# Performance work log

Hardware: AMD Instinct MI355X
Metric: run time of the kernel (lower is better)

Reference implementation:

```python
import jax, jax.numpy as jnp
import numpy as np

B, L, D = 4, 2048, 768
H, K = 12, 9
IPG = D // H  # in-channels per group = head_size = 64
PAD = (K - 1) // 2


def setup_inputs() -> dict:
    key = jax.random.key(0)
    ks = jax.random.split(key, 8)
    s = lambda k, shape, scale: jax.random.normal(k, shape, dtype=jnp.float32) * scale
    return {
        "query": s(ks[0], (B, L, D), 1.0),
        "dw_w": s(ks[1], (D, 1, K), 0.1),          # depthwise Conv1d weight, no bias
        "pw_w": s(ks[2], (H, IPG, IPG), 0.05),     # grouped 1x1 conv [head, out_pg, in_pg]
        "pw_b": s(ks[3], (D,), 0.02),
        "ak_w": s(ks[4], (H, K, IPG), 0.05),       # conv_attn_kernel grouped 1x1 [head, K, in_pg]
        "ak_b": s(ks[5], (H * K,), 0.02),
        "pt_w": s(ks[6], (D, D), 0.02),            # conv_attn_point Linear weight [out, in]
        "pt_b": s(ks[7], (D,), 0.02),
    }


def _sdconv(query, dw_w, pw_w, pw_b, ak_w, ak_b, pt_w, pt_b):
    b, l, d = query.shape
    # SeparableConv1d: depthwise conv (groups=D, kernel K, padding PAD, no bias)
    x = query.transpose(0, 2, 1)  # [B, D, L]
    dw = jax.lax.conv_general_dilated(
        x, dw_w, window_strides=(1,), padding=[(PAD, PAD)],
        feature_group_count=d, dimension_numbers=("NCH", "OIH", "NCH"))  # [B, D, L]
    # grouped pointwise conv (groups=H, kernel 1)
    dwg = dw.reshape(b, H, IPG, l)
    pw = jnp.einsum("bhil,hoi->bhol", dwg, pw_w).reshape(b, d, l) + pw_b[None, :, None]
    key_conv_attn = pw.transpose(0, 2, 1)  # [B, L, D]
    # stride == 1 path: elementwise gate with query
    conv_attn = key_conv_attn * query  # [B, L, D]
    # conv_attn_kernel: grouped 1x1 conv D -> H*K (per head: IPG -> K)
    ca = conv_attn.reshape(b, l, H, IPG)
    kern = jnp.einsum("blhi,hki->blhk", ca, ak_w) + ak_b.reshape(H, K)  # [B, L, H, K]
    w = jax.nn.softmax(kern, axis=-1)  # softmax over kernel positions
    # conv_attn_point linear on value (= query here)
    v = query @ pt_w.T + pt_b  # [B, L, D]
    # unfold: local windows of size K around each position
    vp = jnp.pad(v, ((0, 0), (PAD, PAD), (0, 0)))
    idx = jnp.arange(l)[:, None] + jnp.arange(K)[None, :]  # [L, K]
    win = vp[:, idx]  # [B, L, K, D]
    winh = win.reshape(b, l, K, H, IPG)
    out = jnp.einsum("blkhd,blhk->blhd", winh, w).reshape(b, l, d)
    return out


def reference(query, dw_w, pw_w, pw_b, ak_w, ak_b, pt_w, pt_b):
    return _sdconv(query, dw_w, pw_w, pw_b, ak_w, ak_b, pt_w, pt_b)
```

## Files before the change

### kernel.cpp

```cpp
#include <hip/hip_runtime.h>
#include <math.h>

#define NB 4
#define NL 2048
#define ND 768
#define NH 12
#define NK 9
#define NIPG 64
#define NPAD 4
#define LT 16

typedef __attribute__((ext_vector_type(8))) short s16x8;
typedef __attribute__((ext_vector_type(4))) float f32x4;

__device__ __forceinline__ unsigned short f2bf(float f) {
  unsigned int u = __float_as_uint(f);
  unsigned int r = (u + 0x7FFFu + ((u >> 16) & 1u)) >> 16;
  return (unsigned short)r;
}
__device__ __forceinline__ float bf2f(unsigned short s) {
  return __uint_as_float(((unsigned int)s) << 16);
}

__device__ __forceinline__ void gload16(const void* g, void* l) {
  __builtin_amdgcn_global_load_lds((const __attribute__((address_space(1))) void*)g,
                                   (__attribute__((address_space(3))) void*)l,
                                   16, 0, 0);
}

__global__ __launch_bounds__(256) void f32_to_bf16(const float* __restrict__ src,
                                                   unsigned short* __restrict__ dst,
                                                   int n4) {
  int i = blockIdx.x * 256 + threadIdx.x;
  const int stride = gridDim.x * 256;
  for (; i < n4; i += stride) {
    float4 f = ((const float4*)src)[i];
    ushort4 o;
    o.x = f2bf(f.x); o.y = f2bf(f.y); o.z = f2bf(f.z); o.w = f2bf(f.w);
    ((ushort4*)dst)[i] = o;
  }
}

__global__ __launch_bounds__(256) void prep_w(const float* __restrict__ pw_w,
                                              const float* __restrict__ ak_w,
                                              unsigned short* __restrict__ pwb,
                                              unsigned short* __restrict__ akp) {
  const int t = blockIdx.x * 256 + threadIdx.x;
  if (t < NH * NIPG * NIPG) pwb[t] = f2bf(pw_w[t]);
  if (t < NH * 16 * NIPG) {
    const int h = t >> 10;
    const int r = t & 1023;
    const int k = r >> 6;
    const int i = r & 63;
    akp[t] = (k < NK) ? f2bf(ak_w[((size_t)h * NK + k) * NIPG + i]) : (unsigned short)0;
  }
}

__global__ __launch_bounds__(256) void gemm_v(const unsigned short* __restrict__ qb,
                                              const unsigned short* __restrict__ ptb,
                                              const float* __restrict__ bias,
                                              unsigned short* __restrict__ vb) {
  __shared__ unsigned char lds[16384];
  const int t = threadIdx.x;
  const int m0 = blockIdx.x * 128;
  const int n0 = blockIdx.y * 128;
  const int lane = t & 63;
  const int wv = t >> 6;
  const int wr = wv >> 1, wc = wv & 1;

  const int soff = t * 16;
  const int sr = soff >> 6;
  const int scb = soff & 63;
  const unsigned char* gA0 = (const unsigned char*)qb + (size_t)(m0 + sr) * (ND * 2) + scb;
  const unsigned char* gA1 = gA0 + (size_t)64 * (ND * 2);
  const unsigned char* gB0 = (const unsigned char*)ptb + (size_t)(n0 + sr) * (ND * 2) + scb;
  const unsigned char* gB1 = gB0 + (size_t)64 * (ND * 2);
  unsigned char* lA0 = &lds[soff];
  unsigned char* lA1 = lA0 + 4096;
  unsigned char* lB0 = &lds[8192 + soff];
  unsigned char* lB1 = lB0 + 4096;

  int aoff[4], boff[4];
#pragma unroll
  for (int m = 0; m < 4; ++m)
    aoff[m] = ((wr * 64 + m * 16 + (lane & 15)) * 32 + (lane >> 4) * 8) * 2;
#pragma unroll
  for (int n = 0; n < 4; ++n)
    boff[n] = 8192 + ((wc * 64 + n * 16 + (lane & 15)) * 32 + (lane >> 4) * 8) * 2;

  f32x4 acc[4][4] = {};

  for (int kt = 0; kt < ND / 32; ++kt) {
    const int kb = kt * 64;
    gload16(gA0 + kb, lA0);
    gload16(gA1 + kb, lA1);
    gload16(gB0 + kb, lB0);
    gload16(gB1 + kb, lB1);
    __syncthreads();
    s16x8 av[4], bv[4];
#pragma unroll
    for (int m = 0; m < 4; ++m) av[m] = *(const s16x8*)&lds[aoff[m]];
#pragma unroll
    for (int n = 0; n < 4; ++n) bv[n] = *(const s16x8*)&lds[boff[n]];
#pragma unroll
    for (int m = 0; m < 4; ++m)
#pragma unroll
      for (int n = 0; n < 4; ++n)
        acc[m][n] = __builtin_amdgcn_mfma_f32_16x16x32_bf16(av[m], bv[n], acc[m][n], 0, 0, 0);
    __syncthreads();
  }

#pragma unroll
  for (int m = 0; m < 4; ++m) {
#pragma unroll
    for (int n = 0; n < 4; ++n) {
      const int row = m0 + wr * 64 + m * 16 + (lane >> 4) * 4;
      const int col = n0 + wc * 64 + n * 16 + (lane & 15);
      const float bb = bias[col];
#pragma unroll
      for (int j = 0; j < 4; ++j)
        vb[(size_t)(row + j) * ND + col] = f2bf(acc[m][n][j] + bb);
    }
  }
}

__global__ __launch_bounds__(256) void attn_w(const float* __restrict__ q,
                                              const float* __restrict__ dw_w,
                                              const unsigned short* __restrict__ pwb,
                                              const float* __restrict__ pw_b,
                                              const unsigned short* __restrict__ akp,
                                              const float* __restrict__ ak_b,
                                              float* __restrict__ wout) {
  __shared__ float qs[72][68];
  __shared__ unsigned char ab[8192];
  const int l0 = blockIdx.x * 64;
  const int h  = blockIdx.y;
  const int b  = blockIdx.z;
  const int d0 = h * NIPG;
  const int t  = threadIdx.x;
  const int lane = t & 63;
  const int wv = t >> 6;

  {
    const int sl = t >> 4;
    const int sc = (t & 15) * 4;
    for (int r = sl; r < 72; r += 16) {
      const int l = l0 - NPAD + r;
      float4 val = make_float4(0.f, 0.f, 0.f, 0.f);
      if (l >= 0 && l < NL) val = *(const float4*)&q[((size_t)(b * NL + l)) * ND + d0 + sc];
      *(float4*)&qs[r][sc] = val;
    }
  }
  float dwk[NK];
#pragma unroll
  for (int k = 0; k < NK; ++k) dwk[k] = dw_w[(size_t)(d0 + lane) * NK + k];
  __syncthreads();

  const int lset = wv * 16;
#pragma unroll
  for (int l2 = 0; l2 < 16; ++l2) {
    const int l = lset + l2;
    float s = 0.f;
#pragma unroll
    for (int k = 0; k < NK; ++k) s = fmaf(qs[l + k][lane], dwk[k], s);
    const int byte = ((l * 64 + lane) * 2) ^ ((l & 7) << 4);
    *(unsigned short*)&ab[byte] = f2bf(s);
  }
  __syncthreads();

  const int fr = lane & 15;
  const int fq = lane >> 4;

  s16x8 av0, av1;
  {
    const int row = lset + fr;
    const int b0 = ((row * 64 + fq * 8) * 2)      ^ ((row & 7) << 4);
    const int b1 = ((row * 64 + 32 + fq * 8) * 2) ^ ((row & 7) << 4);
    av0 = *(const s16x8*)&ab[b0];
    av1 = *(const s16x8*)&ab[b1];
  }
  const unsigned short* pwh = pwb + (size_t)h * NIPG * NIPG;
  f32x4 accp[4];
#pragma unroll
  for (int n = 0; n < 4; ++n) {
    accp[n] = (f32x4){0.f, 0.f, 0.f, 0.f};
    const int o = n * 16 + fr;
    s16x8 bv0 = *(const s16x8*)&pwh[o * 64 + fq * 8];
    s16x8 bv1 = *(const s16x8*)&pwh[o * 64 + 32 + fq * 8];
    accp[n] = __builtin_amdgcn_mfma_f32_16x16x32_bf16(av0, bv0, accp[n], 0, 0, 0);
    accp[n] = __builtin_amdgcn_mfma_f32_16x16x32_bf16(av1, bv1, accp[n], 0, 0, 0);
  }
  __syncthreads();

#pragma unroll
  for (int n = 0; n < 4; ++n) {
    const int o = n * 16 + fr;
    const float pb = pw_b[d0 + o];
#pragma unroll
    for (int j = 0; j < 4; ++j) {
      const int row = lset + fq * 4 + j;
      const float ca = (accp[n][j] + pb) * qs[row + NPAD][o];
      const int byte = ((row * 64 + o) * 2) ^ ((row & 7) << 4);
      *(unsigned short*)&ab[byte] = f2bf(ca);
    }
  }
  __syncthreads();

  f32x4 acck = (f32x4){0.f, 0.f, 0.f, 0.f};
  {
    const int row = lset + fr;
    const int b0 = ((row * 64 + fq * 8) * 2)      ^ ((row & 7) << 4);
    const int b1 = ((row * 64 + 32 + fq * 8) * 2) ^ ((row & 7) << 4);
    s16x8 a0 = *(const s16x8*)&ab[b0];
    s16x8 a1 = *(const s16x8*)&ab[b1];
    const unsigned short* akh = akp + (size_t)h * 16 * NIPG;
    s16x8 b0v = *(const s16x8*)&akh[fr * 64 + fq * 8];
    s16x8 b1v = *(const s16x8*)&akh[fr * 64 + 32 + fq * 8];
    acck = __builtin_amdgcn_mfma_f32_16x16x32_bf16(a0, b0v, acck, 0, 0, 0);
    acck = __builtin_amdgcn_mfma_f32_16x16x32_bf16(a1, b1v, acck, 0, 0, 0);
  }

  const bool kvalid = fr < NK;
  const float akbv = kvalid ? ak_b[h * NK + fr] : 0.f;
#pragma unroll
  for (int j = 0; j < 4; ++j) {
    float val = acck[j] + akbv;
    float mv = kvalid ? val : -3.4e38f;
#pragma unroll
    for (int mm = 1; mm < 16; mm <<= 1) mv = fmaxf(mv, __shfl_xor(mv, mm));
    const float e = kvalid ? __expf(val - mv) : 0.f;
    float ssum = e;
#pragma unroll
    for (int mm = 1; mm < 16; mm <<= 1) ssum += __shfl_xor(ssum, mm);
    if (kvalid) {
      const int row = l0 + lset + fq * 4 + j;
      wout[(((size_t)(b * NL + row)) * NH + h) * NK + fr] = e / ssum;
    }
  }
}

__global__ __launch_bounds__(192) void sdconv_out(const unsigned short* __restrict__ v,
                                                  const float* __restrict__ w,
                                                  float* __restrict__ out) {
  const int b  = blockIdx.y;
  const int l0 = blockIdx.x * LT;
  const int t  = threadIdx.x;
  const int d  = t * 4;
  const int h  = t >> 4;
  const size_t vbase = (size_t)b * NL * ND + d;

  float4 win[NK];
#pragma unroll
  for (int k = 0; k < NK; ++k) {
    const int r = l0 - NPAD + k;
    if (r >= 0 && r < NL) {
      ushort4 u = *(const ushort4*)&v[vbase + (size_t)r * ND];
      win[k] = make_float4(bf2f(u.x), bf2f(u.y), bf2f(u.z), bf2f(u.w));
    } else {
      win[k] = make_float4(0.f, 0.f, 0.f, 0.f);
    }
  }
#pragma unroll
  for (int l2 = 0; l2 < LT; ++l2) {
    const int l = l0 + l2;
    const float* wp = &w[(((size_t)(b * NL + l)) * NH + h) * NK];
    float4 acc = make_float4(0.f, 0.f, 0.f, 0.f);
#pragma unroll
    for (int k = 0; k < NK; ++k) {
      const float wk = wp[k];
      acc.x = fmaf(wk, win[k].x, acc.x);
      acc.y = fmaf(wk, win[k].y, acc.y);
      acc.z = fmaf(wk, win[k].z, acc.z);
      acc.w = fmaf(wk, win[k].w, acc.w);
    }
    *(float4*)&out[(size_t)(b * NL + l) * ND + d] = acc;
#pragma unroll
    for (int k = 0; k < NK - 1; ++k) win[k] = win[k + 1];
    const int rn = l + NPAD + 1;
    if (rn < NL) {
      ushort4 u = *(const ushort4*)&v[vbase + (size_t)rn * ND];
      win[NK - 1] = make_float4(bf2f(u.x), bf2f(u.y), bf2f(u.z), bf2f(u.w));
    } else {
      win[NK - 1] = make_float4(0.f, 0.f, 0.f, 0.f);
    }
  }
}

extern "C" void kernel_launch(void* const* d_in, const int* in_sizes, int n_in,
                              void* d_out, int out_size, void* d_ws, size_t ws_size,
                              hipStream_t stream) {
  const float* query = (const float*)d_in[0];
  const float* dw_w  = (const float*)d_in[1];
  const float* pw_w  = (const float*)d_in[2];
  const float* pw_b  = (const float*)d_in[3];
  const float* ak_w  = (const float*)d_in[4];
  const float* ak_b  = (const float*)d_in[5];
  const float* pt_w  = (const float*)d_in[6];
  const float* pt_b  = (const float*)d_in[7];
  float* out = (float*)d_out;

  unsigned short* v = (unsigned short*)d_ws;
  float* w = (float*)(v + (size_t)NB * NL * ND);
  unsigned short* qb  = (unsigned short*)(w + (size_t)NB * NL * NH * NK);
  unsigned short* ptb = qb + (size_t)NB * NL * ND;
  unsigned short* pwb = ptb + (size_t)ND * ND;
  unsigned short* akp = pwb + (size_t)NH * NIPG * NIPG;

  f32_to_bf16<<<1024, 256, 0, stream>>>(query, qb, NB * NL * ND / 4);
  f32_to_bf16<<<256, 256, 0, stream>>>(pt_w, ptb, ND * ND / 4);
  prep_w<<<192, 256, 0, stream>>>(pw_w, ak_w, pwb, akp);

  dim3 g1(NB * NL / 128, ND / 128, 1);
  gemm_v<<<g1, 256, 0, stream>>>(qb, ptb, pt_b, v);

  dim3 g2(NL / 64, NH, NB);
  attn_w<<<g2, 256, 0, stream>>>(query, dw_w, pwb, pw_b, akp, ak_b, w);

  dim3 g3(NL / LT, NB, 1);
  sdconv_out<<<g3, 192, 0, stream>>>(v, w, out);
}
```

Before: 147.9 us.

## Fuse value GEMM with local-window conv and fold query bf16 cast into attn kernel

The value projection GEMM is merged with the windowed weighted-sum output stage. Each block computes a 128-row tile of v (112 output rows plus an 8-row halo on each side) and stores it in LDS, then applies the 9-tap softmax-weighted conv from LDS. This avoids writing v to global memory and reading it back. The query bf16 conversion moves into attn_w, and the weight casts are merged into one prep kernel, which cuts the launch count from six to three. The GEMM loop is also double-buffered. The costs are the halo rows, which add about 14% redundant GEMM work, and larger LDS use per block.

```diff
diff --git a/kernel.cpp b/kernel.cpp
--- a/kernel.cpp
+++ b/kernel.cpp
@@ -8,7 +8,7 @@
 #define NK 9
 #define NIPG 64
 #define NPAD 4
-#define LT 16
+#define MT 112
 
 typedef __attribute__((ext_vector_type(8))) short s16x8;
 typedef __attribute__((ext_vector_type(4))) float f32x4;
@@ -21,32 +21,29 @@
 __device__ __forceinline__ float bf2f(unsigned short s) {
   return __uint_as_float(((unsigned int)s) << 16);
 }
-
 __device__ __forceinline__ void gload16(const void* g, void* l) {
   __builtin_amdgcn_global_load_lds((const __attribute__((address_space(1))) void*)g,
                                    (__attribute__((address_space(3))) void*)l,
                                    16, 0, 0);
 }
 
-__global__ __launch_bounds__(256) void f32_to_bf16(const float* __restrict__ src,
-                                                   unsigned short* __restrict__ dst,
-                                                   int n4) {
-  int i = blockIdx.x * 256 + threadIdx.x;
-  const int stride = gridDim.x * 256;
-  for (; i < n4; i += stride) {
-    float4 f = ((const float4*)src)[i];
-    ushort4 o;
-    o.x = f2bf(f.x); o.y = f2bf(f.y); o.z = f2bf(f.z); o.w = f2bf(f.w);
-    ((ushort4*)dst)[i] = o;
-  }
-}
-
-__global__ __launch_bounds__(256) void prep_w(const float* __restrict__ pw_w,
-                                              const float* __restrict__ ak_w,
-                                              unsigned short* __restrict__ pwb,
-                                              unsigned short* __restrict__ akp) {
+__global__ __launch_bounds__(256) void prep(const float* __restrict__ pt_w,
+                                            const float* __restrict__ pw_w,
+                                            const float* __restrict__ ak_w,
+                                            unsigned short* __restrict__ ptb,
+                                            unsigned short* __restrict__ pwb,
+                                            unsigned short* __restrict__ akp) {
   const int t = blockIdx.x * 256 + threadIdx.x;
-  if (t < NH * NIPG * NIPG) pwb[t] = f2bf(pw_w[t]);
+  if (t < ND * ND / 4) {
+    float4 f = ((const float4*)pt_w)[t];
+    ushort4 o; o.x = f2bf(f.x); o.y = f2bf(f.y); o.z = f2bf(f.z); o.w = f2bf(f.w);
+    ((ushort4*)ptb)[t] = o;
+  }
+  if (t < NH * NIPG * NIPG / 4) {
+    float4 f = ((const float4*)pw_w)[t];
+    ushort4 o; o.x = f2bf(f.x); o.y = f2bf(f.y); o.z = f2bf(f.z); o.w = f2bf(f.w);
+    ((ushort4*)pwb)[t] = o;
+  }
   if (t < NH * 16 * NIPG) {
     const int h = t >> 10;
     const int r = t & 1023;
@@ -56,81 +53,14 @@
   }
 }
 
-__global__ __launch_bounds__(256) void gemm_v(const unsigned short* __restrict__ qb,
-                                              const unsigned short* __restrict__ ptb,
-                                              const float* __restrict__ bias,
-                                              unsigned short* __restrict__ vb) {
-  __shared__ unsigned char lds[16384];
-  const int t = threadIdx.x;
-  const int m0 = blockIdx.x * 128;
-  const int n0 = blockIdx.y * 128;
-  const int lane = t & 63;
-  const int wv = t >> 6;
-  const int wr = wv >> 1, wc = wv & 1;
-
-  const int soff = t * 16;
-  const int sr = soff >> 6;
-  const int scb = soff & 63;
-  const unsigned char* gA0 = (const unsigned char*)qb + (size_t)(m0 + sr) * (ND * 2) + scb;
-  const unsigned char* gA1 = gA0 + (size_t)64 * (ND * 2);
-  const unsigned char* gB0 = (const unsigned char*)ptb + (size_t)(n0 + sr) * (ND * 2) + scb;
-  const unsigned char* gB1 = gB0 + (size_t)64 * (ND * 2);
-  unsigned char* lA0 = &lds[soff];
-  unsigned char* lA1 = lA0 + 4096;
-  unsigned char* lB0 = &lds[8192 + soff];
-  unsigned char* lB1 = lB0 + 4096;
-
-  int aoff[4], boff[4];
-#pragma unroll
-  for (int m = 0; m < 4; ++m)
-    aoff[m] = ((wr * 64 + m * 16 + (lane & 15)) * 32 + (lane >> 4) * 8) * 2;
-#pragma unroll
-  for (int n = 0; n < 4; ++n)
-    boff[n] = 8192 + ((wc * 64 + n * 16 + (lane & 15)) * 32 + (lane >> 4) * 8) * 2;
-
-  f32x4 acc[4][4] = {};
-
-  for (int kt = 0; kt < ND / 32; ++kt) {
-    const int kb = kt * 64;
-    gload16(gA0 + kb, lA0);
-    gload16(gA1 + kb, lA1);
-    gload16(gB0 + kb, lB0);
-    gload16(gB1 + kb, lB1);
-    __syncthreads();
-    s16x8 av[4], bv[4];
-#pragma unroll
-    for (int m = 0; m < 4; ++m) av[m] = *(const s16x8*)&lds[aoff[m]];
-#pragma unroll
-    for (int n = 0; n < 4; ++n) bv[n] = *(const s16x8*)&lds[boff[n]];
-#pragma unroll
-    for (int m = 0; m < 4; ++m)
-#pragma unroll
-      for (int n = 0; n < 4; ++n)
-        acc[m][n] = __builtin_amdgcn_mfma_f32_16x16x32_bf16(av[m], bv[n], acc[m][n], 0, 0, 0);
-    __syncthreads();
-  }
-
-#pragma unroll
-  for (int m = 0; m < 4; ++m) {
-#pragma unroll
-    for (int n = 0; n < 4; ++n) {
-      const int row = m0 + wr * 64 + m * 16 + (lane >> 4) * 4;
-      const int col = n0 + wc * 64 + n * 16 + (lane & 15);
-      const float bb = bias[col];
-#pragma unroll
-      for (int j = 0; j < 4; ++j)
-        vb[(size_t)(row + j) * ND + col] = f2bf(acc[m][n][j] + bb);
-    }
-  }
-}
-
 __global__ __launch_bounds__(256) void attn_w(const float* __restrict__ q,
                                               const float* __restrict__ dw_w,
                                               const unsigned short* __restrict__ pwb,
                                               const float* __restrict__ pw_b,
                                               const unsigned short* __restrict__ akp,
                                               const float* __restrict__ ak_b,
-                                              float* __restrict__ wout) {
+                                              float* __restrict__ wout,
+                                              unsigned short* __restrict__ qb) {
   __shared__ float qs[72][68];
   __shared__ unsigned char ab[8192];
   const int l0 = blockIdx.x * 64;
@@ -149,6 +79,11 @@
       float4 val = make_float4(0.f, 0.f, 0.f, 0.f);
       if (l >= 0 && l < NL) val = *(const float4*)&q[((size_t)(b * NL + l)) * ND + d0 + sc];
       *(float4*)&qs[r][sc] = val;
+      if (r >= NPAD && r < NPAD + 64) {
+        ushort4 ub;
+        ub.x = f2bf(val.x); ub.y = f2bf(val.y); ub.z = f2bf(val.z); ub.w = f2bf(val.w);
+        *(ushort4*)&qb[((size_t)(b * NL + l)) * ND + d0 + sc] = ub;
+      }
     }
   }
   float dwk[NK];
@@ -239,49 +174,118 @@
   }
 }
 
-__global__ __launch_bounds__(192) void sdconv_out(const unsigned short* __restrict__ v,
-                                                  const float* __restrict__ w,
-                                                  float* __restrict__ out) {
-  const int b  = blockIdx.y;
-  const int l0 = blockIdx.x * LT;
-  const int t  = threadIdx.x;
-  const int d  = t * 4;
-  const int h  = t >> 4;
-  const size_t vbase = (size_t)b * NL * ND + d;
-
+__global__ __launch_bounds__(256) void gemm_conv(const unsigned short* __restrict__ qb,
+                                                 const unsigned short* __restrict__ ptb,
+                                                 const float* __restrict__ bias,
+                                                 const float* __restrict__ w,
+                                                 float* __restrict__ out) {
+  __shared__ unsigned char lds[33792];
+  const int t = threadIdx.x;
+  const long mo = (long)blockIdx.x * MT;
+  const int n0 = blockIdx.y * 128;
+  const int lane = t & 63;
+  const int wv = t >> 6;
+  const int wr = wv >> 1, wc = wv & 1;
+  const int fr = lane & 15;
+  const int fq = lane >> 4;
+
+  const int soff = t * 16;
+  const int sr = soff >> 6;
+  const int scb = soff & 63;
+  const unsigned char* gA0 = (const unsigned char*)qb + (mo - 8 + sr) * (long)(ND * 2) + scb;
+  const unsigned char* gA1 = gA0 + (long)64 * (ND * 2);
+  const unsigned char* gB0 = (const unsigned char*)ptb + (size_t)(n0 + sr) * (ND * 2) + scb;
+  const unsigned char* gB1 = gB0 + (size_t)64 * (ND * 2);
+
+  int aoff[4], boff[4];
+#pragma unroll
+  for (int m = 0; m < 4; ++m)
+    aoff[m] = ((wr * 64 + m * 16 + fr) * 32 + fq * 8) * 2;
+#pragma unroll
+  for (int n = 0; n < 4; ++n)
+    boff[n] = 8192 + ((wc * 64 + n * 16 + fr) * 32 + fq * 8) * 2;
+
+#define STAGE(kt, buf)                                             \
+  do {                                                             \
+    const long kb_ = (long)(kt) * 64;                              \
+    unsigned char* base_ = &lds[(buf) * 16384];                    \
+    gload16(gA0 + kb_, base_ + soff);                              \
+    gload16(gA1 + kb_, base_ + 4096 + soff);                       \
+    gload16(gB0 + kb_, base_ + 8192 + soff);                       \
+    gload16(gB1 + kb_, base_ + 12288 + soff);                      \
+  } while (0)
+
+  f32x4 acc[4][4] = {};
+  STAGE(0, 0);
+  __syncthreads();
+  for (int kt = 0; kt < ND / 32; ++kt) {
+    const int cur = kt & 1;
+    if (kt + 1 < ND / 32) STAGE(kt + 1, cur ^ 1);
+    const unsigned char* bb = &lds[cur * 16384];
+    s16x8 av[4], bv[4];
+#pragma unroll
+    for (int m = 0; m < 4; ++m) av[m] = *(const s16x8*)&bb[aoff[m]];
+#pragma unroll
+    for (int n = 0; n < 4; ++n) bv[n] = *(const s16x8*)&bb[boff[n]];
+#pragma unroll
+    for (int m = 0; m < 4; ++m)
+#pragma unroll
+      for (int n = 0; n < 4; ++n)
+        acc[m][n] = __builtin_amdgcn_mfma_f32_16x16x32_bf16(av[m], bv[n], acc[m][n], 0, 0, 0);
+    __syncthreads();
+  }
+#undef STAGE
+
+  unsigned short* vt = (unsigned short*)lds;
+#pragma unroll
+  for (int m = 0; m < 4; ++m) {
+#pragma unroll
+    for (int n = 0; n < 4; ++n) {
+      const int rb = wr * 64 + m * 16 + fq * 4;
+      const int cc = wc * 64 + n * 16 + fr;
+      const float bbv = bias[n0 + cc];
+#pragma unroll
+      for (int j = 0; j < 4; ++j)
+        vt[(rb + j) * 132 + cc] = f2bf(acc[m][n][j] + bbv);
+    }
+  }
+  __syncthreads();
+
+  const int cq = (t & 31) * 4;
+  const int r0 = 8 + (t >> 5) * 14;
+  const int h = (n0 + cq) >> 6;
   float4 win[NK];
 #pragma unroll
   for (int k = 0; k < NK; ++k) {
-    const int r = l0 - NPAD + k;
-    if (r >= 0 && r < NL) {
-      ushort4 u = *(const ushort4*)&v[vbase + (size_t)r * ND];
-      win[k] = make_float4(bf2f(u.x), bf2f(u.y), bf2f(u.z), bf2f(u.w));
-    } else {
-      win[k] = make_float4(0.f, 0.f, 0.f, 0.f);
-    }
-  }
-#pragma unroll
-  for (int l2 = 0; l2 < LT; ++l2) {
-    const int l = l0 + l2;
-    const float* wp = &w[(((size_t)(b * NL + l)) * NH + h) * NK];
-    float4 acc = make_float4(0.f, 0.f, 0.f, 0.f);
-#pragma unroll
-    for (int k = 0; k < NK; ++k) {
-      const float wk = wp[k];
-      acc.x = fmaf(wk, win[k].x, acc.x);
-      acc.y = fmaf(wk, win[k].y, acc.y);
-      acc.z = fmaf(wk, win[k].z, acc.z);
-      acc.w = fmaf(wk, win[k].w, acc.w);
-    }
-    *(float4*)&out[(size_t)(b * NL + l) * ND + d] = acc;
-#pragma unroll
-    for (int k = 0; k < NK - 1; ++k) win[k] = win[k + 1];
-    const int rn = l + NPAD + 1;
-    if (rn < NL) {
-      ushort4 u = *(const ushort4*)&v[vbase + (size_t)rn * ND];
+    ushort4 u = *(const ushort4*)&vt[(r0 - 4 + k) * 132 + cq];
+    win[k] = make_float4(bf2f(u.x), bf2f(u.y), bf2f(u.z), bf2f(u.w));
+  }
+#pragma unroll
+  for (int i = 0; i < 14; ++i) {
+    const int r = r0 + i;
+    const long g = mo + r - 8;
+    if (g < (long)NB * NL) {
+      const int l = (int)(g & (NL - 1));
+      const float* wp = &w[((size_t)g * NH + h) * NK];
+      float4 a = make_float4(0.f, 0.f, 0.f, 0.f);
+#pragma unroll
+      for (int k = 0; k < NK; ++k) {
+        const int lk = l + k - NPAD;
+        if (lk >= 0 && lk < NL) {
+          const float wk = wp[k];
+          a.x = fmaf(wk, win[k].x, a.x);
+          a.y = fmaf(wk, win[k].y, a.y);
+          a.z = fmaf(wk, win[k].z, a.z);
+          a.w = fmaf(wk, win[k].w, a.w);
+        }
+      }
+      *(float4*)&out[(size_t)g * ND + n0 + cq] = a;
+    }
+    if (i < 13) {
+#pragma unroll
+      for (int k = 0; k < NK - 1; ++k) win[k] = win[k + 1];
+      ushort4 u = *(const ushort4*)&vt[(r + 5) * 132 + cq];
       win[NK - 1] = make_float4(bf2f(u.x), bf2f(u.y), bf2f(u.z), bf2f(u.w));
-    } else {
-      win[NK - 1] = make_float4(0.f, 0.f, 0.f, 0.f);
     }
   }
 }
@@ -299,23 +303,17 @@
   const float* pt_b  = (const float*)d_in[7];
   float* out = (float*)d_out;
 
-  unsigned short* v = (unsigned short*)d_ws;
-  float* w = (float*)(v + (size_t)NB * NL * ND);
+  float* w = (float*)d_ws;
   unsigned short* qb  = (unsigned short*)(w + (size_t)NB * NL * NH * NK);
   unsigned short* ptb = qb + (size_t)NB * NL * ND;
   unsigned short* pwb = ptb + (size_t)ND * ND;
   unsigned short* akp = pwb + (size_t)NH * NIPG * NIPG;
 
-  f32_to_bf16<<<1024, 256, 0, stream>>>(query, qb, NB * NL * ND / 4);
-  f32_to_bf16<<<256, 256, 0, stream>>>(pt_w, ptb, ND * ND / 4);
-  prep_w<<<192, 256, 0, stream>>>(pw_w, ak_w, pwb, akp);
-
-  dim3 g1(NB * NL / 128, ND / 128, 1);
-  gemm_v<<<g1, 256, 0, stream>>>(qb, ptb, pt_b, v);
+  prep<<<ND * ND / 4 / 256, 256, 0, stream>>>(pt_w, pw_w, ak_w, ptb, pwb, akp);
 
   dim3 g2(NL / 64, NH, NB);
-  attn_w<<<g2, 256, 0, stream>>>(query, dw_w, pwb, pw_b, akp, ak_b, w);
-
-  dim3 g3(NL / LT, NB, 1);
-  sdconv_out<<<g3, 192, 0, stream>>>(v, w, out);
-}
+  attn_w<<<g2, 256, 0, stream>>>(query, dw_w, pwb, pw_b, akp, ak_b, w, qb);
+
+  dim3 g3((NB * NL + MT - 1) / MT, ND / 128, 1);
+  gemm_conv<<<g3, 256, 0, stream>>>(qb, ptb, pt_b, w, out);
+}
```

New measurement: 148.4 us. Within noise of the previous version (+0.3%).
